# Performance work log

Measured on AMD Instinct MI355X. Metric: run time of the kernel, lower is better.

## Reference

```python
import jax, jax.numpy as jnp
import numpy as np

N, F_IN, F_OUT, K = 4096, 32, 32, 2
NEG_SLOPE = 0.2
MASK_VAL = -9e15


def _sparse_mat(kv, km, density=0.01):
    vals = jax.random.normal(kv, (N, N), dtype=jnp.float32)
    mask = jax.random.uniform(km, (N, N)) < density
    return vals * mask


def setup_inputs() -> dict:
    key = jax.random.key(0)
    ks = jax.random.split(key, 12)
    x = jax.random.normal(ks[0], (N, F_IN), dtype=jnp.float32)
    Ld = _sparse_mat(ks[1], ks[2])
    Lu = _sparse_mat(ks[3], ks[4])
    P = jax.random.normal(ks[5], (N, N), dtype=jnp.float32) / np.sqrt(N)
    W1 = jax.random.normal(ks[6], (K, F_IN, F_OUT), dtype=jnp.float32) * 0.1
    W2 = jax.random.normal(ks[7], (K, F_IN, F_OUT), dtype=jnp.float32) * 0.1
    W0 = jax.random.normal(ks[8], (F_IN, F_OUT), dtype=jnp.float32) * 0.1
    att1 = jax.random.normal(ks[9], (2 * F_OUT * K, 1), dtype=jnp.float32) * 0.1
    att2 = jax.random.normal(ks[10], (2 * F_OUT * K, 1), dtype=jnp.float32) * 0.1
    return {"x": x, "Ld": Ld, "Lu": Lu, "P": P, "W1": W1, "W2": W2,
            "W0": W0, "att1": att1, "att2": att2}


def _branch(x, L, W, att):
    # W: [K, F_in, F_out]; precompute x @ W[k] for all k -> [K, N, F_out]
    Kk, _, Fo = W.shape
    xw = jnp.einsum('nf,kfo->kno', x, W)
    # torch.cat([x@W[k]], dim=1) == transpose+reshape of xw
    xcat = jnp.transpose(xw, (1, 0, 2)).reshape(x.shape[0], Kk * Fo)
    d = Fo * Kk
    e = xcat @ att[:d] + (xcat @ att[d:]).T            # [N, N]
    e = jax.nn.leaky_relu(e, negative_slope=NEG_SLOPE)
    e = jnp.where(L != 0, e, MASK_VAL)
    alpha = jax.nn.softmax(e, axis=1)                   # row softmax, no dropout (eval)
    z = alpha @ xw[0]
    a = alpha
    for k in range(1, Kk):
        a = a @ L
        z = z + a @ xw[k]
    return z


def reference(x, Ld, Lu, P, W1, W2, W0, att1, att2):
    z1 = _branch(x, Ld, W1, att1)
    z2 = _branch(x, Lu, W2, att2)
    x0 = P @ (x @ W0)
    return z1 + z2 + x0
```

## Files before the change

### kernel.cpp

```cpp
#include <hip/hip_runtime.h>
#include <hip/hip_bf16.h>

#define NN 4096
#define CAP 128
#define KS 8

typedef __attribute__((ext_vector_type(8))) short bf16x8;
typedef __attribute__((ext_vector_type(4))) float f32x4;

__device__ __forceinline__ float lrelu(float v) { return v >= 0.f ? v : 0.2f * v; }

__device__ __forceinline__ ushort f2bu(float f) {
    unsigned u = __float_as_uint(f);
    return (ushort)((u + 0x7FFFu + ((u >> 16) & 1u)) >> 16);
}

__global__ __launch_bounds__(256) void k_prep(
    const float* __restrict__ x,
    const float* __restrict__ W1, const float* __restrict__ W2,
    const float* __restrict__ W0,
    const float* __restrict__ att1, const float* __restrict__ att2,
    float* __restrict__ xwA1, float* __restrict__ xwB1,
    float* __restrict__ xwA2, float* __restrict__ xwB2,
    float* __restrict__ a1, float* __restrict__ b1,
    float* __restrict__ a2, float* __restrict__ b2,
    __hip_bfloat16* __restrict__ Bt)
{
    __shared__ float wl[5120];
    __shared__ float xs[256];
    const int t = threadIdx.x;
    for (int i = t; i < 2048; i += 256) { wl[i] = W1[i]; wl[2048 + i] = W2[i]; }
    for (int i = t; i < 1024; i += 256) wl[4096 + i] = W0[i];
    const int rowBase = blockIdx.x * 8;
    xs[t] = x[rowBase * 32 + t];
    __syncthreads();

    const int o = t & 31, r = t >> 5;
    const int row = rowBase + r;
    const float* xr = &xs[r * 32];
    float vA1 = 0.f, vB1 = 0.f, vA2 = 0.f, vB2 = 0.f, v0 = 0.f;
#pragma unroll
    for (int f = 0; f < 32; ++f) {
        const float xv = xr[f];
        vA1 += xv * wl[f * 32 + o];
        vB1 += xv * wl[1024 + f * 32 + o];
        vA2 += xv * wl[2048 + f * 32 + o];
        vB2 += xv * wl[3072 + f * 32 + o];
        v0  += xv * wl[4096 + f * 32 + o];
    }
    xwA1[row * 32 + o] = vA1;
    xwB1[row * 32 + o] = vB1;
    xwA2[row * 32 + o] = vA2;
    xwB2[row * 32 + o] = vB2;
    ((ushort*)Bt)[(size_t)o * NN + row] = f2bu(v0);

    float pa1 = vA1 * att1[o]      + vB1 * att1[32 + o];
    float pb1 = vA1 * att1[64 + o] + vB1 * att1[96 + o];
    float pa2 = vA2 * att2[o]      + vB2 * att2[32 + o];
    float pb2 = vA2 * att2[64 + o] + vB2 * att2[96 + o];
#pragma unroll
    for (int m = 1; m <= 16; m <<= 1) {
        pa1 += __shfl_xor(pa1, m); pb1 += __shfl_xor(pb1, m);
        pa2 += __shfl_xor(pa2, m); pb2 += __shfl_xor(pb2, m);
    }
    if (o == 0) { a1[row] = pa1; b1[row] = pb1; a2[row] = pa2; b2[row] = pb2; }
}

__global__ __launch_bounds__(256) void k_scan(
    const float* __restrict__ Ld, const float* __restrict__ Lu,
    const float* __restrict__ xwB1, const float* __restrict__ xwB2,
    const float* __restrict__ xwA1, const float* __restrict__ xwA2,
    int* __restrict__ csr, int* __restrict__ cntArr,
    float* __restrict__ u1, float* __restrict__ u2)
{
    const int row = blockIdx.x;
    const int br  = blockIdx.y;
    const float* L   = br ? Lu : Ld;
    const float* xwB = br ? xwB2 : xwB1;
    const float* xwA = br ? xwA2 : xwA1;
    int*   csrB = csr + (size_t)br * NN * CAP;
    int*   cntB = cntArr + br * NN;
    float* u    = br ? u2 : u1;

    __shared__ int   sidx[CAP];
    __shared__ float sval[CAP];
    __shared__ int   wcnt[16];
    __shared__ float red[256];
    const int t = threadIdx.x;
    const int lane = t & 63, w = t >> 6;

    const float4* L4 = (const float4*)(L + (size_t)row * NN);
    float4 v[4];
#pragma unroll
    for (int it = 0; it < 4; ++it) v[it] = L4[it * 256 + t];

    const unsigned long long lt = (1ull << lane) - 1ull;

    int tots[4];
#pragma unroll
    for (int it = 0; it < 4; ++it) {
        const unsigned long long m0 = __ballot(v[it].x != 0.f);
        const unsigned long long m1 = __ballot(v[it].y != 0.f);
        const unsigned long long m2 = __ballot(v[it].z != 0.f);
        const unsigned long long m3 = __ballot(v[it].w != 0.f);
        tots[it] = __popcll(m0) + __popcll(m1) + __popcll(m2) + __popcll(m3);
    }
    if (lane == 0) {
        int4 tv; tv.x = tots[0]; tv.y = tots[1]; tv.z = tots[2]; tv.w = tots[3];
        *(int4*)&wcnt[w * 4] = tv;
    }
    __syncthreads();

    const int4 ca = *(const int4*)&wcnt[0];
    const int4 cb = *(const int4*)&wcnt[4];
    const int4 cc = *(const int4*)&wcnt[8];
    const int4 cd = *(const int4*)&wcnt[12];
    const int cs[16] = {ca.x, ca.y, ca.z, ca.w, cb.x, cb.y, cb.z, cb.w,
                        cc.x, cc.y, cc.z, cc.w, cd.x, cd.y, cd.z, cd.w};
    int total = 0;
#pragma unroll
    for (int k2 = 0; k2 < 16; ++k2) total += cs[k2];
    int base = 0;
#pragma unroll
    for (int k2 = 0; k2 < 16; ++k2) base += (k2 < (w << 2)) ? cs[k2] : 0;

    const int cnt  = min(total, CAP);
    const int cp16 = min((cnt + 15) & ~15, CAP);

#pragma unroll
    for (int it = 0; it < 4; ++it) {
        const float vx = v[it].x, vy = v[it].y, vz = v[it].z, vw = v[it].w;
        const unsigned long long m0 = __ballot(vx != 0.f);
        const unsigned long long m1 = __ballot(vy != 0.f);
        const unsigned long long m2 = __ballot(vz != 0.f);
        const unsigned long long m3 = __ballot(vw != 0.f);
        const int p0 = __popcll(m0), p1 = __popcll(m1), p2 = __popcll(m2);
        const int c0 = (it * 256 + t) * 4;
        int s;
        s = base + __popcll(m0 & lt);
        if (vx != 0.f && s < CAP) { sidx[s] = c0;     sval[s] = vx; }
        s = base + p0 + __popcll(m1 & lt);
        if (vy != 0.f && s < CAP) { sidx[s] = c0 + 1; sval[s] = vy; }
        s = base + p0 + p1 + __popcll(m2 & lt);
        if (vz != 0.f && s < CAP) { sidx[s] = c0 + 2; sval[s] = vz; }
        s = base + p0 + p1 + p2 + __popcll(m3 & lt);
        if (vw != 0.f && s < CAP) { sidx[s] = c0 + 3; sval[s] = vw; }
        base += p0 + p1 + p2 + __popcll(m3);
    }
    if (t >= cnt && t < cp16) { sidx[t] = 0; sval[t] = 0.f; }
    __syncthreads();

    if (t < cp16) csrB[(size_t)row * CAP + t] = sidx[t];
    if (t == 0)   cntB[row] = cnt;

    const int o = t & 31, g = t >> 5;
    float acc = 0.f;
    const int nPair = cp16 >> 4;
    if (nPair > 0) {
        int   iA0 = sidx[g],      iA1 = sidx[g + 8];
        float vA0 = sval[g],      vA1 = sval[g + 8];
        float xA0 = xwB[(size_t)iA0 * 32 + o];
        float xA1 = xwB[(size_t)iA1 * 32 + o];
        for (int j = 1; j < nPair; ++j) {
            const int sB = g + 16 * j;
            const int   iB0 = sidx[sB],  iB1 = sidx[sB + 8];
            const float vB0 = sval[sB],  vB1 = sval[sB + 8];
            const float xB0 = xwB[(size_t)iB0 * 32 + o];
            const float xB1 = xwB[(size_t)iB1 * 32 + o];
            acc += vA0 * xA0 + vA1 * xA1;
            vA0 = vB0; xA0 = xB0; vA1 = vB1; xA1 = xB1;
        }
        acc += vA0 * xA0 + vA1 * xA1;
    }
    red[t] = acc;
    __syncthreads();
    if (t < 32) {
        float tot2 = 0.f;
#pragma unroll
        for (int g2 = 0; g2 < 8; ++g2) tot2 += red[g2 * 32 + t];
        u[(size_t)row * 32 + t] = tot2 + xwA[(size_t)row * 32 + t];
    }
}

__global__ __launch_bounds__(256) void k_attn(
    const int* __restrict__ csr, const int* __restrict__ cntArr,
    const float* __restrict__ a1, const float* __restrict__ b1,
    const float* __restrict__ a2, const float* __restrict__ b2,
    const float* __restrict__ u1, const float* __restrict__ u2,
    float* __restrict__ z1, float* __restrict__ z2)
{
    const int br = blockIdx.y;
    const int* csrB = csr + (size_t)br * NN * CAP;
    const int* cntB = cntArr + br * NN;
    const float* aA = br ? a2 : a1;
    const float* bA = br ? b2 : b1;
    const float* U  = br ? u2 : u1;
    float* z = br ? z2 : z1;

    __shared__ float sw[4 * CAP];
    __shared__ int   sci[4 * CAP];
    const int w = threadIdx.x >> 6, lane = threadIdx.x & 63;
    const int row = blockIdx.x * 4 + w;
    const int cnt = cntB[row];
    const int cp16 = min((cnt + 15) & ~15, CAP);
    const float ai = aA[row];
    const int* ci = csrB + (size_t)row * CAP;
    float* swg = sw + w * CAP;
    int*   scg = sci + w * CAP;

    int id0 = 0, id1 = 0;
    if (lane < cp16)      id0 = ci[lane];
    if (lane + 64 < cp16) id1 = ci[lane + 64];
    float e0 = (lane < cnt)      ? lrelu(ai + bA[id0]) : -1e30f;
    float e1 = (lane + 64 < cnt) ? lrelu(ai + bA[id1]) : -1e30f;
    float lmax = fmaxf(e0, e1);
#pragma unroll
    for (int m = 1; m <= 32; m <<= 1) lmax = fmaxf(lmax, __shfl_xor(lmax, m));
    const float w0 = __expf(e0 - lmax), w1 = __expf(e1 - lmax);
    float ssum = w0 + w1;
#pragma unroll
    for (int m = 1; m <= 32; m <<= 1) ssum += __shfl_xor(ssum, m);
    swg[lane] = w0; swg[lane + 64] = w1;
    scg[lane] = id0; scg[lane + 64] = id1;

    const int o = lane & 31, h = lane >> 5;
    float acc = 0.f;
    const int nb = cp16 >> 3;
    if (cnt > 0) {
        float wgA[4], uvA[4];
#pragma unroll
        for (int q = 0; q < 4; ++q) {
            const int s = h + 2 * q;
            wgA[q] = swg[s];
            uvA[q] = U[(size_t)scg[s] * 32 + o];
        }
        for (int j = 1; j < nb; ++j) {
            float wgB[4], uvB[4];
#pragma unroll
            for (int q = 0; q < 4; ++q) {
                const int s = h + 8 * j + 2 * q;
                wgB[q] = swg[s];
                uvB[q] = U[(size_t)scg[s] * 32 + o];
            }
#pragma unroll
            for (int q = 0; q < 4; ++q) acc += wgA[q] * uvA[q];
#pragma unroll
            for (int q = 0; q < 4; ++q) { wgA[q] = wgB[q]; uvA[q] = uvB[q]; }
        }
#pragma unroll
        for (int q = 0; q < 4; ++q) acc += wgA[q] * uvA[q];
    }
    acc += __shfl_xor(acc, 32);
    if (lane < 32) z[(size_t)row * 32 + o] = (cnt > 0) ? acc / ssum : 0.f;
}

__global__ __launch_bounds__(256) void k_pgemm(
    const float* __restrict__ P, const ushort* __restrict__ Bt,
    float* __restrict__ partial)
{
    __shared__ ushort sA[2][16 * 64 * 8];
    __shared__ ushort sB[2][8 * 64 * 8];
    const int t = threadIdx.x;
    const int row0 = blockIdx.x * 64;
    const int ks = blockIdx.y;
    const float4*  P4  = (const float4*)P;
    const ushort4* Bt4 = (const ushort4*)Bt;

    const int lane = t & 63, w = t >> 6;

    f32x4 acc0 = {0.f, 0.f, 0.f, 0.f};
    f32x4 acc1 = {0.f, 0.f, 0.f, 0.f};

    auto stageA = [&](int c, int buf) {
        const int kc4 = (ks * 512 + c * 128) >> 2;
#pragma unroll
        for (int j = 0; j < 8; ++j) {
            const int i = t + 256 * j;
            const int row = i >> 5, q = i & 31;
            const float4 v = P4[(size_t)(row0 + row) * 1024 + kc4 + q];
            ushort4 u;
            u.x = f2bu(v.x); u.y = f2bu(v.y); u.z = f2bu(v.z); u.w = f2bu(v.w);
            const int wi = row >> 4, m = row & 15;
            const int kk = q >> 3, quad = (q >> 1) & 3, jj = q & 1;
            *(ushort4*)&sA[buf][(((wi * 4 + kk) * 64) + quad * 16 + m) * 8 + jj * 4] = u;
        }
    };
    auto stageB = [&](int c, int buf) {
        const int kc4 = (ks * 512 + c * 128) >> 2;
#pragma unroll
        for (int j = 0; j < 4; ++j) {
            const int i = t + 256 * j;
            const int o = i >> 5, q = i & 31;
            const ushort4 u = Bt4[(size_t)o * 1024 + kc4 + q];
            const int nt = o >> 4, n = o & 15;
            const int kk = q >> 3, quad = (q >> 1) & 3, jj = q & 1;
            *(ushort4*)&sB[buf][(((kk * 2 + nt) * 64) + quad * 16 + n) * 8 + jj * 4] = u;
        }
    };
    auto compute = [&](int buf) {
        const ushort* pa = &sA[buf][(w * 4) * 64 * 8 + lane * 8];
        const ushort* pb = &sB[buf][lane * 8];
#pragma unroll
        for (int kk = 0; kk < 4; ++kk) {
            const bf16x8 a  = *(const bf16x8*)(pa + kk * 512);
            const bf16x8 b0 = *(const bf16x8*)(pb + kk * 1024);
            const bf16x8 b1 = *(const bf16x8*)(pb + kk * 1024 + 512);
            acc0 = __builtin_amdgcn_mfma_f32_16x16x32_bf16(a, b0, acc0, 0, 0, 0);
            acc1 = __builtin_amdgcn_mfma_f32_16x16x32_bf16(a, b1, acc1, 0, 0, 0);
        }
    };

    stageA(0, 0); stageB(0, 0);
    __syncthreads();
    for (int c = 0; c < 4; ++c) {
        if (c < 3) { stageA(c + 1, (c + 1) & 1); stageB(c + 1, (c + 1) & 1); }
        compute(c & 1);
        __syncthreads();
    }

    const int m = lane & 15, quad = lane >> 4;
    float* out = partial + ((size_t)ks * NN + row0 + w * 16 + quad * 4) * 32;
#pragma unroll
    for (int r = 0; r < 4; ++r) {
        out[r * 32 + m]      = acc0[r];
        out[r * 32 + 16 + m] = acc1[r];
    }
}

__global__ __launch_bounds__(256) void k_combine(
    const float4* __restrict__ z1, const float4* __restrict__ z2,
    const float4* __restrict__ partial, float4* __restrict__ out)
{
    const int i = blockIdx.x * 256 + threadIdx.x;
    const float4 a = z1[i], b = z2[i];
    float rx = a.x + b.x, ry = a.y + b.y, rz = a.z + b.z, rw = a.w + b.w;
#pragma unroll
    for (int p = 0; p < KS; ++p) {
        const float4 c = partial[p * 32768 + i];
        rx += c.x; ry += c.y; rz += c.z; rw += c.w;
    }
    float4 rr; rr.x = rx; rr.y = ry; rr.z = rz; rr.w = rw;
    out[i] = rr;
}

extern "C" void kernel_launch(void* const* d_in, const int* in_sizes, int n_in,
                              void* d_out, int out_size, void* d_ws, size_t ws_size,
                              hipStream_t stream) {
    (void)in_sizes; (void)n_in; (void)out_size; (void)ws_size;
    const float* x    = (const float*)d_in[0];
    const float* Ld   = (const float*)d_in[1];
    const float* Lu   = (const float*)d_in[2];
    const float* P    = (const float*)d_in[3];
    const float* W1   = (const float*)d_in[4];
    const float* W2   = (const float*)d_in[5];
    const float* W0   = (const float*)d_in[6];
    const float* att1 = (const float*)d_in[7];
    const float* att2 = (const float*)d_in[8];

    float* ws = (float*)d_ws;
    float* xwA1 = ws;
    float* xwB1 = ws + 131072;
    float* xwA2 = ws + 262144;
    float* xwB2 = ws + 393216;
    float* u1   = ws + 524288;
    float* u2   = ws + 655360;
    float* z1   = ws + 786432;
    float* z2   = ws + 917504;
    float* a1   = ws + 1048576;
    float* b1   = ws + 1052672;
    float* a2   = ws + 1056768;
    float* b2   = ws + 1060864;
    float* partial = ws + 1064960;
    __hip_bfloat16* Bt = (__hip_bfloat16*)(ws + 1064960 + KS * 131072);
    int* csr = (int*)(ws + 1064960 + KS * 131072 + 65536);
    int* cnt = (int*)(ws + 1064960 + KS * 131072 + 65536 + 1048576);

    k_prep<<<512, 256, 0, stream>>>(x, W1, W2, W0, att1, att2,
                                    xwA1, xwB1, xwA2, xwB2, a1, b1, a2, b2, Bt);
    k_scan<<<dim3(NN, 2), 256, 0, stream>>>(Ld, Lu, xwB1, xwB2, xwA1, xwA2,
                                            csr, cnt, u1, u2);
    k_attn<<<dim3(NN / 4, 2), 256, 0, stream>>>(csr, cnt, a1, b1, a2, b2,
                                                u1, u2, z1, z2);
    k_pgemm<<<dim3(64, KS), 256, 0, stream>>>(P, (const ushort*)Bt, partial);
    k_combine<<<128, 256, 0, stream>>>((const float4*)z1, (const float4*)z2,
                                       (const float4*)partial, (float4*)d_out);
}
```

Before: 225.8 us.

## Process one sparse row per wavefront in scan kernel, dropping block syncs

The scan kernel now assigns one row per 64-lane wavefront (four rows per block) instead of one row per 256-thread block. Each wave walks the 4096-wide row alone, keeping a running ballot/popcount prefix and a register double buffer of float4 loads, so the cross-wave count exchange and all __syncthreads are gone. Index/value pairs are packed as int2 in shared memory, and the gather-accumulate is reduced with one shuffle rather than a shared-memory reduction. In exchange each wave issues 16 serial row loads and has fewer lanes gathering per row, which may lower memory-level parallelism per row.

```diff
diff --git a/kernel.cpp b/kernel.cpp
--- a/kernel.cpp
+++ b/kernel.cpp
@@ -73,7 +73,8 @@
     int* __restrict__ csr, int* __restrict__ cntArr,
     float* __restrict__ u1, float* __restrict__ u2)
 {
-    const int row = blockIdx.x;
+    const int w = threadIdx.x >> 6, lane = threadIdx.x & 63;
+    const int row = blockIdx.x * 4 + w;
     const int br  = blockIdx.y;
     const float* L   = br ? Lu : Ld;
     const float* xwB = br ? xwB2 : xwB1;
@@ -82,104 +83,64 @@
     int*   cntB = cntArr + br * NN;
     float* u    = br ? u2 : u1;
 
-    __shared__ int   sidx[CAP];
-    __shared__ float sval[CAP];
-    __shared__ int   wcnt[16];
-    __shared__ float red[256];
-    const int t = threadIdx.x;
-    const int lane = t & 63, w = t >> 6;
+    __shared__ int2 sle[4][CAP];
+    int2* se = sle[w];
 
     const float4* L4 = (const float4*)(L + (size_t)row * NN);
-    float4 v[4];
-#pragma unroll
-    for (int it = 0; it < 4; ++it) v[it] = L4[it * 256 + t];
-
     const unsigned long long lt = (1ull << lane) - 1ull;
 
-    int tots[4];
-#pragma unroll
-    for (int it = 0; it < 4; ++it) {
-        const unsigned long long m0 = __ballot(v[it].x != 0.f);
-        const unsigned long long m1 = __ballot(v[it].y != 0.f);
-        const unsigned long long m2 = __ballot(v[it].z != 0.f);
-        const unsigned long long m3 = __ballot(v[it].w != 0.f);
-        tots[it] = __popcll(m0) + __popcll(m1) + __popcll(m2) + __popcll(m3);
-    }
-    if (lane == 0) {
-        int4 tv; tv.x = tots[0]; tv.y = tots[1]; tv.z = tots[2]; tv.w = tots[3];
-        *(int4*)&wcnt[w * 4] = tv;
-    }
-    __syncthreads();
-
-    const int4 ca = *(const int4*)&wcnt[0];
-    const int4 cb = *(const int4*)&wcnt[4];
-    const int4 cc = *(const int4*)&wcnt[8];
-    const int4 cd = *(const int4*)&wcnt[12];
-    const int cs[16] = {ca.x, ca.y, ca.z, ca.w, cb.x, cb.y, cb.z, cb.w,
-                        cc.x, cc.y, cc.z, cc.w, cd.x, cd.y, cd.z, cd.w};
-    int total = 0;
-#pragma unroll
-    for (int k2 = 0; k2 < 16; ++k2) total += cs[k2];
-    int base = 0;
-#pragma unroll
-    for (int k2 = 0; k2 < 16; ++k2) base += (k2 < (w << 2)) ? cs[k2] : 0;
-
-    const int cnt  = min(total, CAP);
+    float4 buf[8];
+#pragma unroll
+    for (int it = 0; it < 8; ++it) buf[it] = L4[it * 64 + lane];
+    int runbase = 0;
+#pragma unroll
+    for (int it = 0; it < 16; ++it) {
+        const float4 vv = buf[it & 7];
+        if (it < 8) buf[it & 7] = L4[(it + 8) * 64 + lane];
+        const unsigned long long m0 = __ballot(vv.x != 0.f);
+        const unsigned long long m1 = __ballot(vv.y != 0.f);
+        const unsigned long long m2 = __ballot(vv.z != 0.f);
+        const unsigned long long m3 = __ballot(vv.w != 0.f);
+        const int p0 = __popcll(m0), p1 = __popcll(m1), p2 = __popcll(m2);
+        const int c0 = (it * 64 + lane) * 4;
+        int s;
+        s = runbase + __popcll(m0 & lt);
+        if (vv.x != 0.f && s < CAP) { int2 e; e.x = c0;     e.y = __float_as_int(vv.x); se[s] = e; }
+        s = runbase + p0 + __popcll(m1 & lt);
+        if (vv.y != 0.f && s < CAP) { int2 e; e.x = c0 + 1; e.y = __float_as_int(vv.y); se[s] = e; }
+        s = runbase + p0 + p1 + __popcll(m2 & lt);
+        if (vv.z != 0.f && s < CAP) { int2 e; e.x = c0 + 2; e.y = __float_as_int(vv.z); se[s] = e; }
+        s = runbase + p0 + p1 + p2 + __popcll(m3 & lt);
+        if (vv.w != 0.f && s < CAP) { int2 e; e.x = c0 + 3; e.y = __float_as_int(vv.w); se[s] = e; }
+        runbase += p0 + p1 + p2 + __popcll(m3);
+    }
+    const int cnt  = min(runbase, CAP);
     const int cp16 = min((cnt + 15) & ~15, CAP);
-
-#pragma unroll
-    for (int it = 0; it < 4; ++it) {
-        const float vx = v[it].x, vy = v[it].y, vz = v[it].z, vw = v[it].w;
-        const unsigned long long m0 = __ballot(vx != 0.f);
-        const unsigned long long m1 = __ballot(vy != 0.f);
-        const unsigned long long m2 = __ballot(vz != 0.f);
-        const unsigned long long m3 = __ballot(vw != 0.f);
-        const int p0 = __popcll(m0), p1 = __popcll(m1), p2 = __popcll(m2);
-        const int c0 = (it * 256 + t) * 4;
-        int s;
-        s = base + __popcll(m0 & lt);
-        if (vx != 0.f && s < CAP) { sidx[s] = c0;     sval[s] = vx; }
-        s = base + p0 + __popcll(m1 & lt);
-        if (vy != 0.f && s < CAP) { sidx[s] = c0 + 1; sval[s] = vy; }
-        s = base + p0 + p1 + __popcll(m2 & lt);
-        if (vz != 0.f && s < CAP) { sidx[s] = c0 + 2; sval[s] = vz; }
-        s = base + p0 + p1 + p2 + __popcll(m3 & lt);
-        if (vw != 0.f && s < CAP) { sidx[s] = c0 + 3; sval[s] = vw; }
-        base += p0 + p1 + p2 + __popcll(m3);
-    }
-    if (t >= cnt && t < cp16) { sidx[t] = 0; sval[t] = 0.f; }
-    __syncthreads();
-
-    if (t < cp16) csrB[(size_t)row * CAP + t] = sidx[t];
-    if (t == 0)   cntB[row] = cnt;
-
-    const int o = t & 31, g = t >> 5;
+    {
+        const int s = cnt + lane;
+        if (s < cp16) { int2 e; e.x = 0; e.y = 0; se[s] = e; }
+    }
+
+    if (lane < cp16)      csrB[(size_t)row * CAP + lane]      = se[lane].x;
+    if (lane + 64 < cp16) csrB[(size_t)row * CAP + lane + 64] = se[lane + 64].x;
+    if (lane == 0) cntB[row] = cnt;
+
+    const int o = lane & 31, g = lane >> 5;
     float acc = 0.f;
-    const int nPair = cp16 >> 4;
-    if (nPair > 0) {
-        int   iA0 = sidx[g],      iA1 = sidx[g + 8];
-        float vA0 = sval[g],      vA1 = sval[g + 8];
-        float xA0 = xwB[(size_t)iA0 * 32 + o];
-        float xA1 = xwB[(size_t)iA1 * 32 + o];
-        for (int j = 1; j < nPair; ++j) {
-            const int sB = g + 16 * j;
-            const int   iB0 = sidx[sB],  iB1 = sidx[sB + 8];
-            const float vB0 = sval[sB],  vB1 = sval[sB + 8];
-            const float xB0 = xwB[(size_t)iB0 * 32 + o];
-            const float xB1 = xwB[(size_t)iB1 * 32 + o];
-            acc += vA0 * xA0 + vA1 * xA1;
-            vA0 = vB0; xA0 = xB0; vA1 = vB1; xA1 = xB1;
-        }
-        acc += vA0 * xA0 + vA1 * xA1;
-    }
-    red[t] = acc;
-    __syncthreads();
-    if (t < 32) {
-        float tot2 = 0.f;
-#pragma unroll
-        for (int g2 = 0; g2 < 8; ++g2) tot2 += red[g2 * 32 + t];
-        u[(size_t)row * 32 + t] = tot2 + xwA[(size_t)row * 32 + t];
-    }
+    const int nb = cp16 >> 3;
+    for (int j = 0; j < nb; ++j) {
+        float wv[4], xv[4];
+#pragma unroll
+        for (int q = 0; q < 4; ++q) {
+            const int2 e = se[8 * j + 2 * q + g];
+            wv[q] = __int_as_float(e.y);
+            xv[q] = xwB[(size_t)e.x * 32 + o];
+        }
+#pragma unroll
+        for (int q = 0; q < 4; ++q) acc += wv[q] * xv[q];
+    }
+    acc += __shfl_xor(acc, 32);
+    if (lane < 32) u[(size_t)row * 32 + o] = acc + xwA[(size_t)row * 32 + o];
 }
 
 __global__ __launch_bounds__(256) void k_attn(
@@ -377,8 +338,8 @@
 
     k_prep<<<512, 256, 0, stream>>>(x, W1, W2, W0, att1, att2,
                                     xwA1, xwB1, xwA2, xwB2, a1, b1, a2, b2, Bt);
-    k_scan<<<dim3(NN, 2), 256, 0, stream>>>(Ld, Lu, xwB1, xwB2, xwA1, xwA2,
-                                            csr, cnt, u1, u2);
+    k_scan<<<dim3(NN / 4, 2), 256, 0, stream>>>(Ld, Lu, xwB1, xwB2, xwA1, xwA2,
+                                                csr, cnt, u1, u2);
     k_attn<<<dim3(NN / 4, 2), 256, 0, stream>>>(csr, cnt, a1, b1, a2, b2,
                                                 u1, u2, z1, z2);
     k_pgemm<<<dim3(64, KS), 256, 0, stream>>>(P, (const ushort*)Bt, partial);
```

After: 230.6 us. 2.1% more time.
